# Kernel tuning notes

Measured on AMD Instinct MI355X. Metric: run time of the kernel, lower is better.

Reference implementation:

```python
import jax, jax.numpy as jnp
import numpy as np

# Dimensions: B jets, P max particles, C coords, F features, K neighbors,
# H hidden units, O MLP output dim. Edge feature dim E = 2*(C+F).
B, P, C, F, K, H, O = 256, 128, 2, 7, 16, 128, 256
E = 2 * (C + F)
BIG = 1e9  # distance assigned to invalid (padded) neighbors


def setup_inputs() -> dict:
    key = jax.random.key(0)
    k1, k2, k3, k4 = jax.random.split(key, 4)
    raw = jax.random.normal(k1, (B, P, C + F), dtype=jnp.float32)
    # per-jet particle counts in [K+2, P]; padding is contiguous at the end
    lengths = jax.random.randint(k2, (B,), K + 2, P + 1)
    mask = (jnp.arange(P)[None, :] < lengths[:, None]).astype(jnp.float32)  # [B,P]
    # zero out padded rows and append mask as the last column (as the layer expects)
    x = jnp.concatenate([raw * mask[..., None], mask[..., None]], axis=-1)  # [B,P,C+F+1]
    W1 = jax.random.normal(k3, (E, H), dtype=jnp.float32) * (1.0 / np.sqrt(E))
    b1 = jnp.zeros((H,), dtype=jnp.float32)
    W2 = jax.random.normal(k4, (H, O), dtype=jnp.float32) * (1.0 / np.sqrt(H))
    b2 = jnp.zeros((O,), dtype=jnp.float32)
    return {"x": x, "W1": W1, "b1": b1, "W2": W2, "b2": b2}


def reference(x, W1, b1, W2, b2):
    coords = x[..., :C]          # [B,P,C]
    feats = x[..., C:-1]         # [B,P,F]
    mask = x[..., -1]            # [B,P] 1=real particle, 0=padding
    valid = mask > 0

    # --- kNN on coordinates (masked, vectorized over jets) ---
    diff = coords[:, :, None, :] - coords[:, None, :, :]      # [B,P,P,C]
    # squared distance: same ordering as tf.norm, avoids sqrt-at-zero issues
    dist2 = jnp.sum(diff * diff, axis=-1)                      # [B,P,P]
    dist2 = jnp.where(valid[:, None, :], dist2, BIG)           # mask padded neighbors
    _, idx = jax.lax.top_k(-dist2, K + 1)                      # [B,P,K+1]
    idx = idx[..., 1:]                                         # drop self -> [B,P,K]

    # --- gather neighbor coords/features ---
    idx_flat = idx.reshape(B, P * K)
    nbr_c = jnp.take_along_axis(coords, idx_flat[..., None], axis=1).reshape(B, P, K, C)
    nbr_f = jnp.take_along_axis(feats, idx_flat[..., None], axis=1).reshape(B, P, K, F)
    ctr_c = jnp.broadcast_to(coords[:, :, None, :], (B, P, K, C))
    ctr_f = jnp.broadcast_to(feats[:, :, None, :], (B, P, K, F))

    # edge features: [coord_i, feat_i, coord_j - coord_i, feat_j - feat_i]
    edge = jnp.concatenate([ctr_c, ctr_f, nbr_c - ctr_c, nbr_f - ctr_f], axis=-1)  # [B,P,K,E]

    # --- MLP + mean aggregation over neighbors ---
    h = jax.nn.relu(edge @ W1 + b1)   # [B,P,K,H]
    h = jax.nn.relu(h @ W2 + b2)      # [B,P,K,O]
    avg = jnp.mean(h, axis=2)         # [B,P,O]

    # append mask column; zero out padded particles (matches _fix_number_of_particles)
    out = jnp.concatenate([avg, jnp.ones((B, P, 1), avg.dtype)], axis=-1) * mask[..., None]
    return out
```

## Files before the change

kernel.cpp:

```cpp
#include <hip/hip_runtime.h>

#define BB 256
#define PP 128
#define CC 2
#define FF 7
#define KK 16
#define HH 128
#define OO 256
#define EE 18
#define XCH 10
#define BIGD 1000000000.0f
#define GPT 4

typedef __bf16 bf16x8 __attribute__((ext_vector_type(8)));
typedef __bf16 bf16x4 __attribute__((ext_vector_type(4)));
typedef float  f32x4  __attribute__((ext_vector_type(4)));

__global__ __launch_bounds__(256) void knn_kernel(const float* __restrict__ x,
                                                  int* __restrict__ idx_out) {
    const int tid = threadIdx.x;
    const int lane = tid & 63;
    const int p = blockIdx.x * 4 + (tid >> 6);
    const int b = p >> 7;
    const int i = p & (PP - 1);
    const float* xb = x + (size_t)b * PP * XCH;

    if (xb[i * XCH + (XCH - 1)] <= 0.0f) return;

    const float cix = xb[i * XCH + 0];
    const float ciy = xb[i * XCH + 1];

    const int j0 = lane, j1 = lane + 64;
    float d0, d1;
    {
        const float2 c0 = *(const float2*)(xb + j0 * XCH);
        float m0 = xb[j0 * XCH + (XCH - 1)];
        float dx = cix - c0.x, dy = ciy - c0.y;
        d0 = __fadd_rn(__fmul_rn(dx, dx), __fmul_rn(dy, dy));
        if (m0 <= 0.0f || j0 == i) d0 = BIGD;
    }
    {
        const float2 c1 = *(const float2*)(xb + j1 * XCH);
        float m1 = xb[j1 * XCH + (XCH - 1)];
        float dx = cix - c1.x, dy = ciy - c1.y;
        d1 = __fadd_rn(__fmul_rn(dx, dx), __fmul_rn(dy, dy));
        if (m1 <= 0.0f || j1 == i) d1 = BIGD;
    }

    const unsigned long long key0 =
        ((unsigned long long)__float_as_uint(d0) << 7) | (unsigned)j0;
    const unsigned long long key1 =
        ((unsigned long long)__float_as_uint(d1) << 7) | (unsigned)j1;

    unsigned long long A0 = ~0ull, A1 = ~0ull, W0 = 0ull, W1 = 0ull;
    int need = KK;
#pragma unroll 1
    for (int bp = 37; bp >= 0; --bp) {
        const unsigned long long z0 = A0 & __ballot(((key0 >> bp) & 1ull) == 0ull);
        const unsigned long long z1 = A1 & __ballot(((key1 >> bp) & 1ull) == 0ull);
        const int c = __popcll(z0) + __popcll(z1);
        if (c == need) { W0 |= z0; W1 |= z1; need = 0; A0 = A1 = 0ull; break; }
        if (c > need) {
            A0 = z0; A1 = z1;
        } else {
            W0 |= z0; W1 |= z1; need -= c;
            A0 &= ~z0; A1 &= ~z1;
        }
    }
    W0 |= A0; W1 |= A1;

    unsigned int mb0 = __builtin_amdgcn_mbcnt_lo((unsigned)(W0 & 0xffffffffull), 0u);
    mb0 = __builtin_amdgcn_mbcnt_hi((unsigned)(W0 >> 32), mb0);
    unsigned int mb1 = __builtin_amdgcn_mbcnt_lo((unsigned)(W1 & 0xffffffffull), 0u);
    mb1 = __builtin_amdgcn_mbcnt_hi((unsigned)(W1 >> 32), mb1);
    const int base1 = __popcll(W0);

    int* op = idx_out + (size_t)p * KK;
    if ((W0 >> lane) & 1ull) op[mb0] = j0;
    if ((W1 >> lane) & 1ull) op[base1 + mb1] = j1;
}

__global__ __launch_bounds__(256) void pack_w_kernel(const float* __restrict__ W1,
                                                     const float* __restrict__ W2,
                                                     __bf16* __restrict__ W2p,
                                                     __bf16* __restrict__ W1p) {
    const int t = blockIdx.x * 256 + threadIdx.x;
    if (t < 32768) {
        const int j  = t & 7;
        const int l  = (t >> 3) & 63;
        const int ks = (t >> 9) & 3;
        const int ct = t >> 11;
        const int row = ks * 32 + ((l >> 4) * 8) + j;
        const int col = ct * 16 + (l & 15);
        W2p[t] = (__bf16)W2[row * OO + col];
    } else {
        const int t2 = t - 32768;
        const int j  = t2 & 7;
        const int l  = (t2 >> 3) & 63;
        const int nt = t2 >> 9;
        const int k  = ((l >> 4) * 8) + j;
        const int n  = nt * 16 + (l & 15);
        W1p[t2] = (k < EE) ? (__bf16)W1[k * HH + n] : (__bf16)0.0f;
    }
}

__global__ __launch_bounds__(256, 4) void mlp_kernel(const float* __restrict__ x,
                                                     const int* __restrict__ knn,
                                                     const __bf16* __restrict__ W1p,
                                                     const float* __restrict__ b1,
                                                     const __bf16* __restrict__ W2p,
                                                     const float* __restrict__ b2,
                                                     float* __restrict__ out) {
    __shared__ __bf16 sh1A[16 * 64 * 8];
    __shared__ float  sb1[HH];
    __shared__ float  sb2[OO];
    __shared__ float  smask[GPT];

    const int tid = threadIdx.x;
    const int lane = tid & 63;
    const int w = tid >> 6;
    const int quad = lane >> 4;
    const int lcol = lane & 15;

    const int pbase = blockIdx.x * GPT;
    const int bidx = pbase >> 7;
    const int i0 = pbase & (PP - 1);
    const float* xb = x + (size_t)bidx * PP * XCH;
    float* outrow = out + (size_t)pbase * (OO + 1);

    if (tid < HH) sb1[tid] = b1[tid];
    sb2[tid] = b2[tid];
    if (tid < GPT) smask[tid] = xb[(i0 + tid) * XCH + (XCH - 1)];
    __syncthreads();

    const bool allmasked =
        (smask[0] == 0.0f) & (smask[1] == 0.0f) & (smask[2] == 0.0f) & (smask[3] == 0.0f);
    if (allmasked) {
        for (int o = tid; o < GPT * (OO + 1); o += 256) outrow[o] = 0.0f;
        return;
    }

    const int i = i0 + w;
    int jn = knn[(size_t)(pbase + w) * KK + lcol];
    jn = (jn < 0) ? 0 : (jn > PP - 1 ? PP - 1 : jn);
    const float* ci = xb + i * XCH;
    const float* cj = xb + jn * XCH;
    const float2 a01 = *(const float2*)(ci + 0);
    const float2 a23 = *(const float2*)(ci + 2);
    const float2 a45 = *(const float2*)(ci + 4);
    const float2 a67 = *(const float2*)(ci + 6);
    const float  a8  = ci[8];
    const float2 n01 = *(const float2*)(cj + 0);
    const float2 n23 = *(const float2*)(cj + 2);
    const float2 n45 = *(const float2*)(cj + 4);
    const float2 n67 = *(const float2*)(cj + 6);
    const float  n8  = cj[8];

    float v[8];
#pragma unroll
    for (int e = 0; e < 8; ++e) v[e] = 0.0f;
    if (quad == 0) {
        v[0] = a01.x; v[1] = a01.y; v[2] = a23.x; v[3] = a23.y;
        v[4] = a45.x; v[5] = a45.y; v[6] = a67.x; v[7] = a67.y;
    } else if (quad == 1) {
        v[0] = a8;
        v[1] = n01.x - a01.x; v[2] = n01.y - a01.y;
        v[3] = n23.x - a23.x; v[4] = n23.y - a23.y;
        v[5] = n45.x - a45.x; v[6] = n45.y - a45.y;
        v[7] = n67.x - a67.x;
    } else if (quad == 2) {
        v[0] = n67.y - a67.y;
        v[1] = n8 - a8;
    }

    bf16x8 ef;
#pragma unroll
    for (int e = 0; e < 8; ++e) ef[e] = (__bf16)v[e];

    bf16x8 wf[8];
#pragma unroll
    for (int nt = 0; nt < 8; ++nt)
        wf[nt] = *(const bf16x8*)&W1p[(size_t)((nt * 64 + lane) * 8)];

    const f32x4 z4 = {0.0f, 0.0f, 0.0f, 0.0f};
    f32x4 h[8];
#pragma unroll
    for (int nt = 0; nt < 8; ++nt)
        h[nt] = __builtin_amdgcn_mfma_f32_16x16x32_bf16(wf[nt], ef, z4, 0, 0, 0);

#pragma unroll
    for (int nt = 0; nt < 8; ++nt) {
        const int ks = nt >> 1;
        const int lp = (((nt * 2 + (quad >> 1)) & 3) << 4) | lcol;
        bf16x4 hv;
#pragma unroll
        for (int r = 0; r < 4; ++r) {
            const int m = nt * 16 + quad * 4 + r;
            hv[r] = (__bf16)fmaxf(h[nt][r] + sb1[m], 0.0f);
        }
        *(bf16x4*)&sh1A[((ks * 4 + w) * 64 + lp) * 8 + (quad & 1) * 4] = hv;
    }
    __syncthreads();

    f32x4 acc[GPT][4];
#pragma unroll
    for (int g = 0; g < GPT; ++g)
#pragma unroll
        for (int ct = 0; ct < 4; ++ct) acc[g][ct] = z4;

#pragma unroll
    for (int ks = 0; ks < 4; ++ks) {
        bf16x8 af[GPT], bfr[4];
#pragma unroll
        for (int g = 0; g < GPT; ++g)
            af[g] = *(const bf16x8*)&sh1A[((ks * 4 + g) * 64 + lane) * 8];
#pragma unroll
        for (int ct = 0; ct < 4; ++ct)
            bfr[ct] = *(const bf16x8*)&W2p[(size_t)((((w * 4 + ct) * 4 + ks) * 64 + lane) * 8)];
#pragma unroll
        for (int g = 0; g < GPT; ++g)
#pragma unroll
            for (int ct = 0; ct < 4; ++ct)
                acc[g][ct] = __builtin_amdgcn_mfma_f32_16x16x32_bf16(
                    af[g], bfr[ct], acc[g][ct], 0, 0, 0);
    }

    float val[4];
#pragma unroll
    for (int g = 0; g < GPT; ++g) {
#pragma unroll
        for (int ct = 0; ct < 4; ++ct) {
            const int col = w * 64 + ct * 16 + lcol;
            const float bc = sb2[col];
            float s = 0.0f;
#pragma unroll
            for (int r = 0; r < 4; ++r) s += fmaxf(acc[g][ct][r] + bc, 0.0f);
            s += __shfl_xor(s, 16, 64);
            s += __shfl_xor(s, 32, 64);
            if (quad == g) val[ct] = s;
        }
    }
    const float m = smask[quad] * (1.0f / KK);
#pragma unroll
    for (int ct = 0; ct < 4; ++ct)
        outrow[(size_t)quad * (OO + 1) + w * 64 + ct * 16 + lcol] = val[ct] * m;
    if (tid < GPT) outrow[(size_t)tid * (OO + 1) + OO] = smask[tid];

    (void)knn; (void)x;
}

extern "C" void kernel_launch(void* const* d_in, const int* in_sizes, int n_in,
                              void* d_out, int out_size, void* d_ws, size_t ws_size,
                              hipStream_t stream) {
    const float* x  = (const float*)d_in[0];
    const float* W1 = (const float*)d_in[1];
    const float* b1 = (const float*)d_in[2];
    const float* W2 = (const float*)d_in[3];
    const float* b2 = (const float*)d_in[4];
    float* out = (float*)d_out;

    int* knn_idx = (int*)d_ws;
    __bf16* W2p = (__bf16*)((char*)d_ws + 2 * 1024 * 1024);
    __bf16* W1p = (__bf16*)((char*)d_ws + 2 * 1024 * 1024 + 65536);

    knn_kernel<<<(BB * PP) / 4, 256, 0, stream>>>(x, knn_idx);
    pack_w_kernel<<<144, 256, 0, stream>>>(W1, W2, W2p, W1p);

    const int nblocks = (BB * PP) / GPT;
    mlp_kernel<<<nblocks, 256, 0, stream>>>(x, knn_idx, W1p, b1, W2p, b2, out);
}
```

Before: 138.4 us.

## Fuse kNN selection into MLP kernel and shorten radix-select bit loop

Removes the separate kNN kernel and computes the neighbor selection inside the MLP kernel, each wave selecting neighbors for its own particle and passing indices through shared memory. This drops a kernel launch and the global round-trip of the index buffer. The radix select now iterates over the 31 distance bits with early exit and resolves ties on index using fixed lane-mask steps instead of ballots over 38 packed key bits. It adds a block-wide barrier and select work inside the MLP kernel, which could raise register pressure under the launch bound of 4 blocks.

```diff
diff --git a/kernel.cpp b/kernel.cpp
--- a/kernel.cpp
+++ b/kernel.cpp
@@ -15,70 +15,6 @@
 typedef __bf16 bf16x8 __attribute__((ext_vector_type(8)));
 typedef __bf16 bf16x4 __attribute__((ext_vector_type(4)));
 typedef float  f32x4  __attribute__((ext_vector_type(4)));
-
-__global__ __launch_bounds__(256) void knn_kernel(const float* __restrict__ x,
-                                                  int* __restrict__ idx_out) {
-    const int tid = threadIdx.x;
-    const int lane = tid & 63;
-    const int p = blockIdx.x * 4 + (tid >> 6);
-    const int b = p >> 7;
-    const int i = p & (PP - 1);
-    const float* xb = x + (size_t)b * PP * XCH;
-
-    if (xb[i * XCH + (XCH - 1)] <= 0.0f) return;
-
-    const float cix = xb[i * XCH + 0];
-    const float ciy = xb[i * XCH + 1];
-
-    const int j0 = lane, j1 = lane + 64;
-    float d0, d1;
-    {
-        const float2 c0 = *(const float2*)(xb + j0 * XCH);
-        float m0 = xb[j0 * XCH + (XCH - 1)];
-        float dx = cix - c0.x, dy = ciy - c0.y;
-        d0 = __fadd_rn(__fmul_rn(dx, dx), __fmul_rn(dy, dy));
-        if (m0 <= 0.0f || j0 == i) d0 = BIGD;
-    }
-    {
-        const float2 c1 = *(const float2*)(xb + j1 * XCH);
-        float m1 = xb[j1 * XCH + (XCH - 1)];
-        float dx = cix - c1.x, dy = ciy - c1.y;
-        d1 = __fadd_rn(__fmul_rn(dx, dx), __fmul_rn(dy, dy));
-        if (m1 <= 0.0f || j1 == i) d1 = BIGD;
-    }
-
-    const unsigned long long key0 =
-        ((unsigned long long)__float_as_uint(d0) << 7) | (unsigned)j0;
-    const unsigned long long key1 =
-        ((unsigned long long)__float_as_uint(d1) << 7) | (unsigned)j1;
-
-    unsigned long long A0 = ~0ull, A1 = ~0ull, W0 = 0ull, W1 = 0ull;
-    int need = KK;
-#pragma unroll 1
-    for (int bp = 37; bp >= 0; --bp) {
-        const unsigned long long z0 = A0 & __ballot(((key0 >> bp) & 1ull) == 0ull);
-        const unsigned long long z1 = A1 & __ballot(((key1 >> bp) & 1ull) == 0ull);
-        const int c = __popcll(z0) + __popcll(z1);
-        if (c == need) { W0 |= z0; W1 |= z1; need = 0; A0 = A1 = 0ull; break; }
-        if (c > need) {
-            A0 = z0; A1 = z1;
-        } else {
-            W0 |= z0; W1 |= z1; need -= c;
-            A0 &= ~z0; A1 &= ~z1;
-        }
-    }
-    W0 |= A0; W1 |= A1;
-
-    unsigned int mb0 = __builtin_amdgcn_mbcnt_lo((unsigned)(W0 & 0xffffffffull), 0u);
-    mb0 = __builtin_amdgcn_mbcnt_hi((unsigned)(W0 >> 32), mb0);
-    unsigned int mb1 = __builtin_amdgcn_mbcnt_lo((unsigned)(W1 & 0xffffffffull), 0u);
-    mb1 = __builtin_amdgcn_mbcnt_hi((unsigned)(W1 >> 32), mb1);
-    const int base1 = __popcll(W0);
-
-    int* op = idx_out + (size_t)p * KK;
-    if ((W0 >> lane) & 1ull) op[mb0] = j0;
-    if ((W1 >> lane) & 1ull) op[base1 + mb1] = j1;
-}
 
 __global__ __launch_bounds__(256) void pack_w_kernel(const float* __restrict__ W1,
                                                      const float* __restrict__ W2,
@@ -105,7 +41,6 @@
 }
 
 __global__ __launch_bounds__(256, 4) void mlp_kernel(const float* __restrict__ x,
-                                                     const int* __restrict__ knn,
                                                      const __bf16* __restrict__ W1p,
                                                      const float* __restrict__ b1,
                                                      const __bf16* __restrict__ W2p,
@@ -115,6 +50,7 @@
     __shared__ float  sb1[HH];
     __shared__ float  sb2[OO];
     __shared__ float  smask[GPT];
+    __shared__ int    sknn[GPT][KK];
 
     const int tid = threadIdx.x;
     const int lane = tid & 63;
@@ -141,8 +77,76 @@
     }
 
     const int i = i0 + w;
-    int jn = knn[(size_t)(pbase + w) * KK + lcol];
-    jn = (jn < 0) ? 0 : (jn > PP - 1 ? PP - 1 : jn);
+    const float cix = xb[i * XCH + 0];
+    const float ciy = xb[i * XCH + 1];
+
+    const int j0 = lane, j1 = lane + 64;
+    float d0, d1;
+    {
+        const float2 c0 = *(const float2*)(xb + j0 * XCH);
+        const float m0 = xb[j0 * XCH + (XCH - 1)];
+        float dx = cix - c0.x, dy = ciy - c0.y;
+        d0 = __fadd_rn(__fmul_rn(dx, dx), __fmul_rn(dy, dy));
+        if (m0 <= 0.0f || j0 == i) d0 = BIGD;
+    }
+    {
+        const float2 c1 = *(const float2*)(xb + j1 * XCH);
+        const float m1 = xb[j1 * XCH + (XCH - 1)];
+        float dx = cix - c1.x, dy = ciy - c1.y;
+        d1 = __fadd_rn(__fmul_rn(dx, dx), __fmul_rn(dy, dy));
+        if (m1 <= 0.0f || j1 == i) d1 = BIGD;
+    }
+
+    const unsigned d0b = __float_as_uint(d0);
+    const unsigned d1b = __float_as_uint(d1);
+
+    unsigned long long A0 = ~0ull, A1 = ~0ull, W0 = 0ull, W1 = 0ull;
+    int need = KK;
+
+    auto step = [&](unsigned long long m0, unsigned long long m1) {
+        const unsigned long long z0 = A0 & m0;
+        const unsigned long long z1 = A1 & m1;
+        const int c = __popcll(z0) + __popcll(z1);
+        if (c == need) { W0 |= z0; W1 |= z1; A0 = A1 = 0ull; need = 0; }
+        else if (c > need) { A0 = z0; A1 = z1; }
+        else { W0 |= z0; W1 |= z1; need -= c; A0 &= ~z0; A1 &= ~z1; }
+    };
+
+#pragma unroll 1
+    for (int bp = 30; bp >= 0; --bp) {
+        if (need == 0) break;
+        const unsigned long long m0 = __ballot(((d0b >> bp) & 1u) == 0u);
+        const unsigned long long m1 = __ballot(((d1b >> bp) & 1u) == 0u);
+        step(m0, m1);
+    }
+    if (need) step(~0ull, 0ull);
+    {
+        const unsigned long long M5 = 0x00000000FFFFFFFFull;
+        const unsigned long long M4 = 0x0000FFFF0000FFFFull;
+        const unsigned long long M3 = 0x00FF00FF00FF00FFull;
+        const unsigned long long M2 = 0x0F0F0F0F0F0F0F0Full;
+        const unsigned long long M1 = 0x3333333333333333ull;
+        const unsigned long long M0 = 0x5555555555555555ull;
+        if (need) step(M5, M5);
+        if (need) step(M4, M4);
+        if (need) step(M3, M3);
+        if (need) step(M2, M2);
+        if (need) step(M1, M1);
+        if (need) step(M0, M0);
+    }
+    W0 |= A0; W1 |= A1;
+
+    unsigned int mb0 = __builtin_amdgcn_mbcnt_lo((unsigned)(W0 & 0xffffffffull), 0u);
+    mb0 = __builtin_amdgcn_mbcnt_hi((unsigned)(W0 >> 32), mb0);
+    unsigned int mb1 = __builtin_amdgcn_mbcnt_lo((unsigned)(W1 & 0xffffffffull), 0u);
+    mb1 = __builtin_amdgcn_mbcnt_hi((unsigned)(W1 >> 32), mb1);
+    const int base1 = __popcll(W0);
+
+    if ((W0 >> lane) & 1ull) sknn[w][mb0] = j0;
+    if ((W1 >> lane) & 1ull) sknn[w][base1 + mb1] = j1;
+    __syncthreads();
+
+    const int jn = sknn[w][lcol];
     const float* ci = xb + i * XCH;
     const float* cj = xb + jn * XCH;
     const float2 a01 = *(const float2*)(ci + 0);
@@ -245,8 +249,6 @@
     for (int ct = 0; ct < 4; ++ct)
         outrow[(size_t)quad * (OO + 1) + w * 64 + ct * 16 + lcol] = val[ct] * m;
     if (tid < GPT) outrow[(size_t)tid * (OO + 1) + OO] = smask[tid];
-
-    (void)knn; (void)x;
 }
 
 extern "C" void kernel_launch(void* const* d_in, const int* in_sizes, int n_in,
@@ -259,13 +261,11 @@
     const float* b2 = (const float*)d_in[4];
     float* out = (float*)d_out;
 
-    int* knn_idx = (int*)d_ws;
-    __bf16* W2p = (__bf16*)((char*)d_ws + 2 * 1024 * 1024);
-    __bf16* W1p = (__bf16*)((char*)d_ws + 2 * 1024 * 1024 + 65536);
-
-    knn_kernel<<<(BB * PP) / 4, 256, 0, stream>>>(x, knn_idx);
+    __bf16* W2p = (__bf16*)d_ws;
+    __bf16* W1p = (__bf16*)((char*)d_ws + 65536);
+
     pack_w_kernel<<<144, 256, 0, stream>>>(W1, W2, W2p, W1p);
 
     const int nblocks = (BB * PP) / GPT;
-    mlp_kernel<<<nblocks, 256, 0, stream>>>(x, knn_idx, W1p, b1, W2p, b2, out);
+    mlp_kernel<<<nblocks, 256, 0, stream>>>(x, W1p, b1, W2p, b2, out);
 }
```

After: 129.5 us. 6.5% less time.
